# Kernel optimization log

Hardware: AMD Instinct MI355X
Metric: run time of the kernel (lower is better)

Reference implementation:

```python
import jax, jax.numpy as jnp
import numpy as np

N = 32768   # total nodes
P = 1024    # nodes per graph
B = 32      # graphs (N = B*P)
D = 256     # dim_h
H = 8       # num_heads
E = 262144  # edges
BN_EPS = 1e-5


def setup_inputs() -> dict:
    key = jax.random.key(0)
    ks = jax.random.split(key, 24)
    s = 0.05
    x = jax.random.normal(ks[0], (N, D), jnp.float32)
    src = jax.random.randint(ks[1], (E,), 0, N, dtype=jnp.int32)
    dst = (src // P) * P + jax.random.randint(ks[2], (E,), 0, P, dtype=jnp.int32)
    edge_index = jnp.stack([src, dst])  # [2, E], edges within the same graph
    edge_attr = jax.random.normal(ks[3], (E, D), jnp.float32)
    return {
        "x": x,
        "edge_index": edge_index,
        "edge_attr": edge_attr,
        # GINE nn: Linear(D,D) -> ReLU -> Linear(D,D)
        "gin_w1": s * jax.random.normal(ks[4], (D, D)),
        "gin_b1": jnp.zeros((D,)),
        "gin_w2": s * jax.random.normal(ks[5], (D, D)),
        "gin_b2": jnp.zeros((D,)),
        # MultiheadAttention packed in-proj and out-proj
        "in_w": s * jax.random.normal(ks[6], (3 * D, D)),
        "in_b": jnp.zeros((3 * D,)),
        "out_w": s * jax.random.normal(ks[7], (D, D)),
        "out_b": jnp.zeros((D,)),
        # BatchNorm1d affine params (training-mode batch stats)
        "bn1l_g": jnp.ones((D,)) + s * jax.random.normal(ks[8], (D,)),
        "bn1l_b": s * jax.random.normal(ks[9], (D,)),
        "bn1a_g": jnp.ones((D,)) + s * jax.random.normal(ks[10], (D,)),
        "bn1a_b": s * jax.random.normal(ks[11], (D,)),
        # FF block: Linear(D,2D) -> ReLU -> Linear(2D,D)
        "ff_w1": s * jax.random.normal(ks[12], (2 * D, D)),
        "ff_b1": jnp.zeros((2 * D,)),
        "ff_w2": s * jax.random.normal(ks[13], (D, 2 * D)),
        "ff_b2": jnp.zeros((D,)),
        "bn2_g": jnp.ones((D,)) + s * jax.random.normal(ks[14], (D,)),
        "bn2_b": s * jax.random.normal(ks[15], (D,)),
    }


def _batchnorm(x, g, b):
    # BatchNorm1d, training mode: biased batch statistics over the node axis.
    m = jnp.mean(x, axis=0)
    v = jnp.mean((x - m) ** 2, axis=0)
    return g * (x - m) * jax.lax.rsqrt(v + BN_EPS) + b


def reference(x, edge_index, edge_attr, gin_w1, gin_b1, gin_w2, gin_b2,
              in_w, in_b, out_w, out_b, bn1l_g, bn1l_b, bn1a_g, bn1a_b,
              ff_w1, ff_b1, ff_w2, ff_b2, bn2_g, bn2_b):
    h_in = x
    # ---- local branch: GINEConv (eps = 0) ----
    msg = jax.nn.relu(x[edge_index[0]] + edge_attr)          # [E, D]
    aggr = jax.ops.segment_sum(msg, edge_index[1], num_segments=N)
    z = x + aggr                                             # (1+eps)*x_i + sum msg
    h_local = jax.nn.relu(z @ gin_w1.T + gin_b1) @ gin_w2.T + gin_b2
    h_local = _batchnorm(h_in + h_local, bn1l_g, bn1l_b)
    # ---- global branch: dense-batch MHA (equal-size graphs -> full mask) ----
    hd = x.reshape(B, P, D)
    qkv = hd @ in_w.T + in_b                                 # [B, P, 3D]
    q, k, v = jnp.split(qkv, 3, axis=-1)
    dh = D // H
    q = q.reshape(B, P, H, dh).transpose(0, 2, 1, 3)         # [B, H, P, dh]
    k = k.reshape(B, P, H, dh).transpose(0, 2, 1, 3)
    v = v.reshape(B, P, H, dh).transpose(0, 2, 1, 3)
    scores = jnp.einsum("bhqd,bhkd->bhqk", q, k) / np.sqrt(dh)
    attn = jax.nn.softmax(scores, axis=-1)
    o = jnp.einsum("bhqk,bhkd->bhqd", attn, v)               # [B, H, P, dh]
    o = o.transpose(0, 2, 1, 3).reshape(B, P, D) @ out_w.T + out_b
    h_attn = o.reshape(N, D)
    h_attn = _batchnorm(h_in + h_attn, bn1a_g, bn1a_b)
    # ---- combine + FF + norm ----
    h = h_local + h_attn
    ff = jax.nn.relu(h @ ff_w1.T + ff_b1) @ ff_w2.T + ff_b2
    h = _batchnorm(h + ff, bn2_g, bn2_b)
    return h
```

## Files before the change

kernel.cpp:

```cpp
#include <hip/hip_runtime.h>
#include <hip/hip_bf16.h>

constexpr int D = 256;
constexpr int PG = 1024;

typedef __attribute__((ext_vector_type(8))) short bf16x8;
typedef __attribute__((ext_vector_type(4))) float f32x4;

__device__ inline short f2bf(float f) {
    __hip_bfloat16 h = __float2bfloat16(f);
    return *reinterpret_cast<short*>(&h);
}
__device__ inline float bf2f(short s) {
    return __uint_as_float(((unsigned)(unsigned short)s) << 16);
}

__global__ __launch_bounds__(256) void cvt_weights(
    const float* __restrict__ w1, const float* __restrict__ w2,
    const float* __restrict__ w3, const float* __restrict__ w4,
    const float* __restrict__ w5, const float* __restrict__ w6,
    short* __restrict__ out)
{
    int i = blockIdx.x * 256 + threadIdx.x;
    const float* src; int base;
    if (i < 16384)      { if (i < 8192) { src = w1; base = 0; }
                          else          { src = w2; base = 8192; } }
    else if (i < 40960) { src = w3; base = 16384; }
    else if (i < 49152) { src = w4; base = 40960; }
    else if (i < 65536) { src = w5; base = 49152; }
    else                { src = w6; base = 65536; }
    int k = i - base;
    float4 a = ((const float4*)src)[k * 2];
    float4 b = ((const float4*)src)[k * 2 + 1];
    bf16x8 v;
    v[0] = f2bf(a.x); v[1] = f2bf(a.y); v[2] = f2bf(a.z); v[3] = f2bf(a.w);
    v[4] = f2bf(b.x); v[5] = f2bf(b.y); v[6] = f2bf(b.z); v[7] = f2bf(b.w);
    ((bf16x8*)out)[i] = v;
}

__global__ __launch_bounds__(256) void hist_kernel(
    const int* __restrict__ dst, int* __restrict__ cnt, int E)
{
    int e = blockIdx.x * 256 + threadIdx.x;
    if (e < E) atomicAdd(&cnt[dst[e]], 1);
}

__global__ __launch_bounds__(256) void scan_block(
    const int* __restrict__ cnt, int* __restrict__ excl, int* __restrict__ bsum)
{
    __shared__ int sm[256];
    const int t = threadIdx.x;
    const int i = blockIdx.x * 256 + t;
    int v = cnt[i];
    sm[t] = v;
    __syncthreads();
    #pragma unroll
    for (int o = 1; o < 256; o <<= 1) {
        int u = (t >= o) ? sm[t - o] : 0;
        __syncthreads();
        sm[t] += u;
        __syncthreads();
    }
    excl[i] = sm[t] - v;
    if (t == 255) bsum[blockIdx.x] = sm[255];
}

__global__ __launch_bounds__(128) void scan_bsum(int* __restrict__ bsum)
{
    __shared__ int sm[128];
    const int t = threadIdx.x;
    int v = bsum[t];
    sm[t] = v;
    __syncthreads();
    #pragma unroll
    for (int o = 1; o < 128; o <<= 1) {
        int u = (t >= o) ? sm[t - o] : 0;
        __syncthreads();
        sm[t] += u;
        __syncthreads();
    }
    bsum[t] = sm[t] - v;
}

__global__ __launch_bounds__(256) void scan_add(
    const int* __restrict__ excl, const int* __restrict__ bsum,
    int* __restrict__ rowptr, int* __restrict__ ofs)
{
    int i = blockIdx.x * 256 + threadIdx.x;
    int r = excl[i] + bsum[blockIdx.x];
    rowptr[i] = r;
    ofs[i] = r;
}

__global__ __launch_bounds__(256) void scatter_kernel(
    const int* __restrict__ src, const int* __restrict__ dst,
    int* __restrict__ ofs, int* __restrict__ eord, int* __restrict__ esrc, int E)
{
    int e = blockIdx.x * 256 + threadIdx.x;
    if (e >= E) return;
    int d = dst[e];
    int pos = atomicAdd(&ofs[d], 1);
    eord[pos] = e;
    esrc[pos] = src[e];
}

__global__ __launch_bounds__(256) void csr_aggr(
    const float* __restrict__ x, const float* __restrict__ ea,
    const int* __restrict__ rowptr, const int* __restrict__ cnt,
    const int* __restrict__ eord, const int* __restrict__ esrc,
    short* __restrict__ z)
{
    int gid = blockIdx.x * 256 + threadIdx.x;
    int node = gid >> 6;
    int c = (gid & 63) << 2;
    int start = rowptr[node];
    int deg = cnt[node];
    float4 acc = *(const float4*)(x + (size_t)node * D + c);
    for (int i = 0; i < deg; ++i) {
        int e = eord[start + i];
        int s = esrc[start + i];
        float4 xa = *(const float4*)(x + (size_t)s * D + c);
        float4 av = *(const float4*)(ea + (size_t)e * D + c);
        acc.x += fmaxf(xa.x + av.x, 0.f);
        acc.y += fmaxf(xa.y + av.y, 0.f);
        acc.z += fmaxf(xa.z + av.z, 0.f);
        acc.w += fmaxf(xa.w + av.w, 0.f);
    }
    short4 r;
    r.x = f2bf(acc.x); r.y = f2bf(acc.y); r.z = f2bf(acc.z); r.w = f2bf(acc.w);
    *(short4*)(z + (size_t)node * D + c) = r;
}

template<bool XF32, bool RELU, bool ADDF, bool ADDB, bool STATS>
__global__ __launch_bounds__(256) void gemm_mfma(
    const short* __restrict__ X, const float* __restrict__ Xf,
    const short* __restrict__ W, const float* __restrict__ bias,
    const float* __restrict__ addf, const short* __restrict__ addb,
    short* __restrict__ Y, float* __restrict__ st, int K, int M)
{
    __shared__ __align__(16) short Xs[128 * 72];
    __shared__ __align__(16) short Ws[128 * 72];

    const int nbx = gridDim.x;
    const int nwg = nbx * gridDim.y;
    const int bid = blockIdx.y * nbx + blockIdx.x;
    const int cpx = nwg >> 3;
    const int wg  = (bid & 7) * cpx + (bid >> 3);
    const int r0 = (wg / nbx) * 128;
    const int c0 = (wg % nbx) * 128;

    const int t = threadIdx.x, w = t >> 6, l = t & 63;
    const int wr = w >> 1, wc = w & 1, lg = l >> 4, lm = l & 15;
    const int srow = t >> 3;
    const int scol = (t & 7) * 8;

    f32x4 acc[4][4];
    #pragma unroll
    for (int i = 0; i < 4; ++i)
        #pragma unroll
        for (int j = 0; j < 4; ++j)
            acc[i][j] = (f32x4){0.f, 0.f, 0.f, 0.f};

    for (int k0 = 0; k0 < K; k0 += 64) {
        __syncthreads();
        #pragma unroll
        for (int it = 0; it < 4; ++it) {
            int r = it * 32 + srow;
            bf16x8 xv;
            if (XF32) {
                const float* p = Xf + (size_t)(r0 + r) * K + k0 + scol;
                float4 a = *(const float4*)p;
                float4 b = *(const float4*)(p + 4);
                xv[0] = f2bf(a.x); xv[1] = f2bf(a.y); xv[2] = f2bf(a.z); xv[3] = f2bf(a.w);
                xv[4] = f2bf(b.x); xv[5] = f2bf(b.y); xv[6] = f2bf(b.z); xv[7] = f2bf(b.w);
            } else {
                xv = *(const bf16x8*)(X + (size_t)(r0 + r) * K + k0 + scol);
            }
            bf16x8 wv = *(const bf16x8*)(W + (size_t)(c0 + r) * K + k0 + scol);
            *(bf16x8*)&Xs[r * 72 + scol] = xv;
            *(bf16x8*)&Ws[r * 72 + scol] = wv;
        }
        __syncthreads();

        bf16x8 af[4][2], bfr[4][2];
        #pragma unroll
        for (int i = 0; i < 4; ++i)
            #pragma unroll
            for (int ks = 0; ks < 2; ++ks) {
                af[i][ks]  = *(const bf16x8*)&Xs[(wr*64 + i*16 + lm)*72 + ks*32 + lg*8];
                bfr[i][ks] = *(const bf16x8*)&Ws[(wc*64 + i*16 + lm)*72 + ks*32 + lg*8];
            }
        #pragma unroll
        for (int i = 0; i < 4; ++i)
            #pragma unroll
            for (int j = 0; j < 4; ++j) {
                acc[i][j] = __builtin_amdgcn_mfma_f32_16x16x32_bf16(af[i][0], bfr[j][0], acc[i][j], 0, 0, 0);
                acc[i][j] = __builtin_amdgcn_mfma_f32_16x16x32_bf16(af[i][1], bfr[j][1], acc[i][j], 0, 0, 0);
            }
    }

    float s4[4] = {}, q4[4] = {};
    #pragma unroll
    for (int j = 0; j < 4; ++j) {
        int col = c0 + wc*64 + j*16 + lm;
        float bj = bias[col];
        #pragma unroll
        for (int i = 0; i < 4; ++i) {
            #pragma unroll
            for (int r = 0; r < 4; ++r) {
                int row = r0 + wr*64 + i*16 + lg*4 + r;
                size_t off = (size_t)row * M + col;
                float v = acc[i][j][r] + bj;
                if (RELU) v = fmaxf(v, 0.f);
                if (ADDF) v += addf[off];
                if (ADDB) v += bf2f(addb[off]);
                if (STATS) { s4[j] += v; q4[j] = fmaf(v, v, q4[j]); }
                Y[off] = f2bf(v);
            }
        }
    }
    if (STATS) {
        #pragma unroll
        for (int j = 0; j < 4; ++j) {
            s4[j] += __shfl_xor(s4[j], 16); q4[j] += __shfl_xor(q4[j], 16);
            s4[j] += __shfl_xor(s4[j], 32); q4[j] += __shfl_xor(q4[j], 32);
        }
        if (lg == 0) {
            #pragma unroll
            for (int j = 0; j < 4; ++j) {
                int col = c0 + wc*64 + j*16 + lm;
                atomicAdd(&st[col], s4[j]);
                atomicAdd(&st[256 + col], q4[j]);
            }
        }
    }
}

__global__ __launch_bounds__(256) void attn_mfma(
    const short* __restrict__ QKV, short* __restrict__ O)
{
    const int bh = blockIdx.x & 255;
    const int qblk = blockIdx.x >> 8;
    const int b = bh >> 3, h = bh & 7;
    const int t = threadIdx.x, w = t >> 6, l = t & 63;
    const int lg = l >> 4, lm = l & 15;
    const size_t gb = (size_t)b * PG * 768;
    const int q0 = qblk * 128 + w * 32;
    const float rscale = 0.17677669529663687f;

    __shared__ __align__(16) short Ks[64 * 40];
    __shared__ __align__(16) short Vt[32 * 72];
    __shared__ __align__(16) short Ps[4][32 * 72];

    bf16x8 qa[2];
    #pragma unroll
    for (int qt = 0; qt < 2; ++qt)
        qa[qt] = *(const bf16x8*)(QKV + gb + (size_t)(q0 + qt*16 + lm) * 768 + h*32 + lg*8);

    f32x4 acc[2][2];
    #pragma unroll
    for (int qt = 0; qt < 2; ++qt)
        #pragma unroll
        for (int hf = 0; hf < 2; ++hf)
            acc[qt][hf] = (f32x4){0.f, 0.f, 0.f, 0.f};
    float lsum[2][4] = {};

    const int srow = t >> 2;
    const int sq = (t & 3) * 8;

    for (int kt = 0; kt < 16; ++kt) {
        bf16x8 kv = *(const bf16x8*)(QKV + gb + (size_t)(kt*64 + srow) * 768 + 256 + h*32 + sq);
        bf16x8 vv = *(const bf16x8*)(QKV + gb + (size_t)(kt*64 + srow) * 768 + 512 + h*32 + sq);
        *(bf16x8*)&Ks[srow * 40 + sq] = kv;
        #pragma unroll
        for (int j = 0; j < 8; ++j) Vt[(sq + j) * 72 + srow] = vv[j];
        __syncthreads();

        #pragma unroll
        for (int qt = 0; qt < 2; ++qt) {
            #pragma unroll
            for (int s = 0; s < 4; ++s) {
                bf16x8 kf = *(const bf16x8*)&Ks[(s*16 + lm) * 40 + lg*8];
                f32x4 c = (f32x4){0.f, 0.f, 0.f, 0.f};
                c = __builtin_amdgcn_mfma_f32_16x16x32_bf16(qa[qt], kf, c, 0, 0, 0);
                #pragma unroll
                for (int r = 0; r < 4; ++r) {
                    float p = __expf(c[r] * rscale);
                    lsum[qt][r] += p;
                    Ps[w][(qt*16 + lg*4 + r) * 72 + s*16 + lm] = f2bf(p);
                }
            }
        }

        bf16x8 vf[2][2];
        #pragma unroll
        for (int hf = 0; hf < 2; ++hf)
            #pragma unroll
            for (int g = 0; g < 2; ++g)
                vf[hf][g] = *(const bf16x8*)&Vt[(hf*16 + lm) * 72 + g*32 + lg*8];
        #pragma unroll
        for (int qt = 0; qt < 2; ++qt) {
            #pragma unroll
            for (int g = 0; g < 2; ++g) {
                bf16x8 pf = *(const bf16x8*)&Ps[w][(qt*16 + lm) * 72 + g*32 + lg*8];
                #pragma unroll
                for (int hf = 0; hf < 2; ++hf)
                    acc[qt][hf] = __builtin_amdgcn_mfma_f32_16x16x32_bf16(
                        pf, vf[hf][g], acc[qt][hf], 0, 0, 0);
            }
        }
        __syncthreads();
    }

    #pragma unroll
    for (int qt = 0; qt < 2; ++qt) {
        #pragma unroll
        for (int r = 0; r < 4; ++r) {
            float v = lsum[qt][r];
            for (int off = 1; off < 16; off <<= 1) v += __shfl_xor(v, off);
            float inv = 1.0f / v;
            int qrow = q0 + qt*16 + lg*4 + r;
            short* Op = O + ((size_t)b * PG + qrow) * D + h * 32;
            Op[lm]      = f2bf(acc[qt][0][r] * inv);
            Op[16 + lm] = f2bf(acc[qt][1][r] * inv);
        }
    }
}

__global__ __launch_bounds__(256) void bn_combine(
    const short* __restrict__ A, const short* __restrict__ Bq,
    const float* __restrict__ gl, const float* __restrict__ bl,
    const float* __restrict__ ga, const float* __restrict__ ba,
    const float* __restrict__ st, short* __restrict__ H, int n)
{
    const float invN = 1.0f / (float)n;
    size_t i = (size_t)blockIdx.x * 256 + threadIdx.x;
    int c0 = (int)((i & 31) << 3);
    bf16x8 av = ((const bf16x8*)A)[i];
    bf16x8 bv = ((const bf16x8*)Bq)[i];
    bf16x8 o;
    #pragma unroll
    for (int e = 0; e < 8; ++e) {
        int c = c0 + e;
        float m1 = st[c] * invN;
        float v1 = fmaxf(st[256 + c] * invN - m1 * m1, 0.f);
        float m2 = st[512 + c] * invN;
        float v2 = fmaxf(st[768 + c] * invN - m2 * m2, 0.f);
        float y1 = gl[c] * (bf2f(av[e]) - m1) * rsqrtf(v1 + 1e-5f) + bl[c];
        float y2 = ga[c] * (bf2f(bv[e]) - m2) * rsqrtf(v2 + 1e-5f) + ba[c];
        o[e] = f2bf(y1 + y2);
    }
    ((bf16x8*)H)[i] = o;
}

__global__ __launch_bounds__(256) void bn_apply(
    const short* __restrict__ X, const float* __restrict__ g,
    const float* __restrict__ bb, const float* __restrict__ st,
    float* __restrict__ out, int n)
{
    const float invN = 1.0f / (float)n;
    size_t i = (size_t)blockIdx.x * 256 + threadIdx.x;
    int c0 = (int)((i & 31) << 3);
    bf16x8 xv = ((const bf16x8*)X)[i];
    float r[8];
    #pragma unroll
    for (int e = 0; e < 8; ++e) {
        int c = c0 + e;
        float m = st[c] * invN;
        float v = fmaxf(st[256 + c] * invN - m * m, 0.f);
        r[e] = g[c] * (bf2f(xv[e]) - m) * rsqrtf(v + 1e-5f) + bb[c];
    }
    float4 o0 = {r[0], r[1], r[2], r[3]};
    float4 o1 = {r[4], r[5], r[6], r[7]};
    ((float4*)out)[i * 2]     = o0;
    ((float4*)out)[i * 2 + 1] = o1;
}

extern "C" void kernel_launch(void* const* d_in, const int* in_sizes, int n_in,
                              void* d_out, int out_size, void* d_ws, size_t ws_size,
                              hipStream_t stream)
{
    const float* x    = (const float*)d_in[0];
    const int*   ei   = (const int*)d_in[1];
    const float* ea   = (const float*)d_in[2];
    const float* gw1  = (const float*)d_in[3];
    const float* gb1  = (const float*)d_in[4];
    const float* gw2  = (const float*)d_in[5];
    const float* gb2  = (const float*)d_in[6];
    const float* inw  = (const float*)d_in[7];
    const float* inb  = (const float*)d_in[8];
    const float* outw = (const float*)d_in[9];
    const float* outb = (const float*)d_in[10];
    const float* g1l  = (const float*)d_in[11];
    const float* b1l  = (const float*)d_in[12];
    const float* g1a  = (const float*)d_in[13];
    const float* b1a  = (const float*)d_in[14];
    const float* fw1  = (const float*)d_in[15];
    const float* fb1  = (const float*)d_in[16];
    const float* fw2  = (const float*)d_in[17];
    const float* fb2  = (const float*)d_in[18];
    const float* g2   = (const float*)d_in[19];
    const float* b2   = (const float*)d_in[20];
    float* out = (float*)d_out;

    const int N = in_sizes[0] / D;
    const int E = in_sizes[1] / 2;
    const size_t ND = (size_t)N * D;

    short* Bp = (short*)d_ws;
    short* S0 = Bp;
    short* S1 = Bp + ND;
    short* S2 = Bp + 2 * ND;
    short* S3 = Bp + 3 * ND;
    short* S4 = Bp + 4 * ND;
    short* Wb = Bp + 5 * ND;
    short* gw1b = Wb, *gw2b = Wb + 65536, *inwb = Wb + 131072;
    short* outwb = Wb + 327680, *fw1b = Wb + 393216, *fw2b = Wb + 524288;
    float* st = (float*)(Wb + 655360);
    int* cnt    = (int*)(st + 1536);
    int* excl   = cnt + N;
    int* rowptr = excl + N;
    int* ofs    = rowptr + N;
    int* bsum   = ofs + N;
    int* eord   = bsum + 256;
    int* esrc   = eord + E;

    const int GR = N / 128;
    const int EB = (E + 255) / 256;

    cvt_weights<<<320, 256, 0, stream>>>(gw1, gw2, inw, outw, fw1, fw2, Wb);

    hipMemsetAsync(st, 0, (1536 + (size_t)N) * sizeof(int), stream);
    hist_kernel<<<EB, 256, 0, stream>>>(ei + E, cnt, E);
    scan_block<<<N / 256, 256, 0, stream>>>(cnt, excl, bsum);
    scan_bsum<<<1, 128, 0, stream>>>(bsum);
    scan_add<<<N / 256, 256, 0, stream>>>(excl, bsum, rowptr, ofs);
    scatter_kernel<<<EB, 256, 0, stream>>>(ei, ei + E, ofs, eord, esrc, E);

    csr_aggr<<<(N * 64) / 256, 256, 0, stream>>>(x, ea, rowptr, cnt, eord, esrc, S0);
    gemm_mfma<false, true , false, false, false><<<dim3(2, GR), 256, 0, stream>>>(
        S0, nullptr, gw1b, gb1, nullptr, nullptr, S1, nullptr, 256, 256);
    gemm_mfma<false, false, true , false, true ><<<dim3(2, GR), 256, 0, stream>>>(
        S1, nullptr, gw2b, gb2, x, nullptr, S3, st, 256, 256);

    gemm_mfma<true , false, false, false, false><<<dim3(6, GR), 256, 0, stream>>>(
        nullptr, x, inwb, inb, nullptr, nullptr, S0, nullptr, 256, 768);
    attn_mfma<<<(N / PG) * 8 * 8, 256, 0, stream>>>(S0, S4);
    gemm_mfma<false, false, true , false, true ><<<dim3(2, GR), 256, 0, stream>>>(
        S4, nullptr, outwb, outb, x, nullptr, S0, st + 512, 256, 256);

    bn_combine<<<(unsigned)(ND / 8 / 256), 256, 0, stream>>>(
        S3, S0, g1l, b1l, g1a, b1a, st, S1, N);
    gemm_mfma<false, true , false, false, false><<<dim3(4, GR), 256, 0, stream>>>(
        S1, nullptr, fw1b, fb1, nullptr, nullptr, S2, nullptr, 256, 512);
    gemm_mfma<false, false, false, true , true ><<<dim3(2, GR), 256, 0, stream>>>(
        S2, nullptr, fw2b, fb2, nullptr, S1, S4, st + 1024, 512, 256);
    bn_apply<<<(unsigned)(ND / 8 / 256), 256, 0, stream>>>(
        S4, g2, b2, st + 1024, out, N);
}
```

Measured before the change: 403.7 us.

## Prefetch K/V into registers, transpose score MFMA, fold softmax scale into Q projection

```diff
diff --git a/kernel.cpp b/kernel.cpp
--- a/kernel.cpp
+++ b/kernel.cpp
@@ -131,7 +131,7 @@
     *(short4*)(z + (size_t)node * D + c) = r;
 }
 
-template<bool XF32, bool RELU, bool ADDF, bool ADDB, bool STATS>
+template<bool XF32, bool RELU, bool ADDF, bool ADDB, bool STATS, bool SCALEQ>
 __global__ __launch_bounds__(256) void gemm_mfma(
     const short* __restrict__ X, const float* __restrict__ Xf,
     const short* __restrict__ W, const float* __restrict__ bias,
@@ -212,6 +212,7 @@
                 size_t off = (size_t)row * M + col;
                 float v = acc[i][j][r] + bj;
                 if (RELU) v = fmaxf(v, 0.f);
+                if (SCALEQ) { if (col < 256) v *= 0.17677669529663687f; }
                 if (ADDF) v += addf[off];
                 if (ADDB) v += bf2f(addb[off]);
                 if (STATS) { s4[j] += v; q4[j] = fmaf(v, v, q4[j]); }
@@ -246,7 +247,6 @@
     const int lg = l >> 4, lm = l & 15;
     const size_t gb = (size_t)b * PG * 768;
     const int q0 = qblk * 128 + w * 32;
-    const float rscale = 0.17677669529663687f;
 
     __shared__ __align__(16) short Ks[64 * 40];
     __shared__ __align__(16) short Vt[32 * 72];
@@ -263,32 +263,43 @@
         #pragma unroll
         for (int hf = 0; hf < 2; ++hf)
             acc[qt][hf] = (f32x4){0.f, 0.f, 0.f, 0.f};
-    float lsum[2][4] = {};
+    float lsum[2] = {0.f, 0.f};
 
     const int srow = t >> 2;
     const int sq = (t & 3) * 8;
+    const short* Kb = QKV + gb + 256 + h*32 + sq;
+    const short* Vb = QKV + gb + 512 + h*32 + sq;
+
+    bf16x8 kreg = *(const bf16x8*)(Kb + (size_t)srow * 768);
+    bf16x8 vreg = *(const bf16x8*)(Vb + (size_t)srow * 768);
 
     for (int kt = 0; kt < 16; ++kt) {
-        bf16x8 kv = *(const bf16x8*)(QKV + gb + (size_t)(kt*64 + srow) * 768 + 256 + h*32 + sq);
-        bf16x8 vv = *(const bf16x8*)(QKV + gb + (size_t)(kt*64 + srow) * 768 + 512 + h*32 + sq);
-        *(bf16x8*)&Ks[srow * 40 + sq] = kv;
-        #pragma unroll
-        for (int j = 0; j < 8; ++j) Vt[(sq + j) * 72 + srow] = vv[j];
-        __syncthreads();
+        *(bf16x8*)&Ks[srow * 40 + sq] = kreg;
+        #pragma unroll
+        for (int j = 0; j < 8; ++j) Vt[(sq + j) * 72 + srow] = vreg[j];
+        __syncthreads();
+        if (kt < 15) {
+            kreg = *(const bf16x8*)(Kb + (size_t)((kt + 1) * 64 + srow) * 768);
+            vreg = *(const bf16x8*)(Vb + (size_t)((kt + 1) * 64 + srow) * 768);
+        }
+
+        bf16x8 kf[4];
+        #pragma unroll
+        for (int s = 0; s < 4; ++s)
+            kf[s] = *(const bf16x8*)&Ks[(s*16 + lm) * 40 + lg*8];
 
         #pragma unroll
         for (int qt = 0; qt < 2; ++qt) {
             #pragma unroll
             for (int s = 0; s < 4; ++s) {
-                bf16x8 kf = *(const bf16x8*)&Ks[(s*16 + lm) * 40 + lg*8];
                 f32x4 c = (f32x4){0.f, 0.f, 0.f, 0.f};
-                c = __builtin_amdgcn_mfma_f32_16x16x32_bf16(qa[qt], kf, c, 0, 0, 0);
-                #pragma unroll
-                for (int r = 0; r < 4; ++r) {
-                    float p = __expf(c[r] * rscale);
-                    lsum[qt][r] += p;
-                    Ps[w][(qt*16 + lg*4 + r) * 72 + s*16 + lm] = f2bf(p);
-                }
+                c = __builtin_amdgcn_mfma_f32_16x16x32_bf16(kf[s], qa[qt], c, 0, 0, 0);
+                float p0 = __expf(c[0]), p1 = __expf(c[1]);
+                float p2 = __expf(c[2]), p3 = __expf(c[3]);
+                lsum[qt] += (p0 + p1) + (p2 + p3);
+                short4 pk;
+                pk.x = f2bf(p0); pk.y = f2bf(p1); pk.z = f2bf(p2); pk.w = f2bf(p3);
+                *(short4*)&Ps[w][(qt*16 + lm) * 72 + s*16 + lg*4] = pk;
             }
         }
 
@@ -312,13 +323,19 @@
         __syncthreads();
     }
 
+    float red[2];
     #pragma unroll
     for (int qt = 0; qt < 2; ++qt) {
+        float v = lsum[qt];
+        v += __shfl_xor(v, 16);
+        v += __shfl_xor(v, 32);
+        red[qt] = 1.0f / v;
+    }
+    #pragma unroll
+    for (int qt = 0; qt < 2; ++qt) {
         #pragma unroll
         for (int r = 0; r < 4; ++r) {
-            float v = lsum[qt][r];
-            for (int off = 1; off < 16; off <<= 1) v += __shfl_xor(v, off);
-            float inv = 1.0f / v;
+            float inv = __shfl(red[qt], lg*4 + r);
             int qrow = q0 + qt*16 + lg*4 + r;
             short* Op = O + ((size_t)b * PG + qrow) * D + h * 32;
             Op[lm]      = f2bf(acc[qt][0][r] * inv);
@@ -438,22 +455,22 @@
     scatter_kernel<<<EB, 256, 0, stream>>>(ei, ei + E, ofs, eord, esrc, E);
 
     csr_aggr<<<(N * 64) / 256, 256, 0, stream>>>(x, ea, rowptr, cnt, eord, esrc, S0);
-    gemm_mfma<false, true , false, false, false><<<dim3(2, GR), 256, 0, stream>>>(
+    gemm_mfma<false, true , false, false, false, false><<<dim3(2, GR), 256, 0, stream>>>(
         S0, nullptr, gw1b, gb1, nullptr, nullptr, S1, nullptr, 256, 256);
-    gemm_mfma<false, false, true , false, true ><<<dim3(2, GR), 256, 0, stream>>>(
+    gemm_mfma<false, false, true , false, true , false><<<dim3(2, GR), 256, 0, stream>>>(
         S1, nullptr, gw2b, gb2, x, nullptr, S3, st, 256, 256);
 
-    gemm_mfma<true , false, false, false, false><<<dim3(6, GR), 256, 0, stream>>>(
+    gemm_mfma<true , false, false, false, false, true ><<<dim3(6, GR), 256, 0, stream>>>(
         nullptr, x, inwb, inb, nullptr, nullptr, S0, nullptr, 256, 768);
     attn_mfma<<<(N / PG) * 8 * 8, 256, 0, stream>>>(S0, S4);
-    gemm_mfma<false, false, true , false, true ><<<dim3(2, GR), 256, 0, stream>>>(
+    gemm_mfma<false, false, true , false, true , false><<<dim3(2, GR), 256, 0, stream>>>(
         S4, nullptr, outwb, outb, x, nullptr, S0, st + 512, 256, 256);
 
     bn_combine<<<(unsigned)(ND / 8 / 256), 256, 0, stream>>>(
         S3, S0, g1l, b1l, g1a, b1a, st, S1, N);
-    gemm_mfma<false, true , false, false, false><<<dim3(4, GR), 256, 0, stream>>>(
+    gemm_mfma<false, true , false, false, false, false><<<dim3(4, GR), 256, 0, stream>>>(
         S1, nullptr, fw1b, fb1, nullptr, nullptr, S2, nullptr, 256, 512);
-    gemm_mfma<false, false, false, true , true ><<<dim3(2, GR), 256, 0, stream>>>(
+    gemm_mfma<false, false, false, true , true , false><<<dim3(2, GR), 256, 0, stream>>>(
         S2, nullptr, fw2b, fb2, nullptr, S1, S4, st + 1024, 512, 256);
     bn_apply<<<(unsigned)(ND / 8 / 256), 256, 0, stream>>>(
         S4, g2, b2, st + 1024, out, N);
```

After: 390.3 us. 3.3% less time.
